# Performance work log

Hardware: AMD Instinct MI355X
Metric: run time of the kernel (lower is better)

The kernel has to match this reference:

```python
import jax, jax.numpy as jnp
import numpy as np
from jax import lax

BETA = 5.0
THRESHOLD = 20.0

def softplus5(x):
    # torch nn.Softplus(beta=5, threshold=20)
    return jnp.where(BETA * x > THRESHOLD, x, jax.nn.softplus(BETA * x) / BETA)

def setup_inputs() -> dict:
    key = jax.random.key(0)
    k1, k2, k3, k4, k5 = jax.random.split(key, 5)
    B, T, I, H = 128, 256, 1024, 1024
    stdv = 1.0 / np.sqrt(H)
    x = jax.random.normal(k1, (B, T, I), dtype=jnp.float32)
    hidden = jnp.zeros((2, B, H), dtype=jnp.float32)
    Wi = jax.random.uniform(k2, (H, I), dtype=jnp.float32, minval=-stdv, maxval=stdv)
    bi = jax.random.uniform(k3, (H,), dtype=jnp.float32, minval=-stdv, maxval=stdv)
    Wh = jax.random.uniform(k4, (H, H), dtype=jnp.float32, minval=-stdv, maxval=stdv)
    bh = jax.random.uniform(k5, (H,), dtype=jnp.float32, minval=-stdv, maxval=stdv)
    return {"x": x, "hidden": hidden, "Wi": Wi, "bi": bi, "Wh": Wh, "bh": bh}

def reference(x, hidden, Wi, bi, Wh, bh):
    # x: [B, T, I] (batch_first) -> time-major [T, B, I]
    xt = jnp.swapaxes(x, 0, 1)
    T = xt.shape[0]
    # precompute i2h for all steps (one big GEMM)
    pre = jnp.einsum('tbi,hi->tbh', xt, Wi) + bi  # [T, B, H]

    def step(h, p):
        h_next = softplus5(p + h @ Wh.T + bh)
        return h_next, h_next

    _, fwd = lax.scan(step, hidden[0], pre)          # fwd[t]: hidden after step t
    _, bwd = lax.scan(step, hidden[1], pre[::-1])    # bwd[j]: backward hidden at time i = T-1-j
    # bi_outputs appended for i = T-1 ... 0: position t holds cat(outputs[(T-1-t)-16], bwd[t])
    idx = (jnp.arange(T)[::-1] - 16) % T  # Python negative-index wrap of outputs[i-16]
    out = jnp.concatenate([fwd[idx], bwd], axis=-1)  # [T, B, 2H]
    return jnp.swapaxes(out, 0, 1)                   # [B, T, 2H]
```

## Files before the change

### kernel.cpp

```cpp
#include <hip/hip_runtime.h>
#include <stddef.h>

using short8 = __attribute__((ext_vector_type(8))) short;
using f32x4  = __attribute__((ext_vector_type(4))) float;
using f32x16 = __attribute__((ext_vector_type(16))) float;
using u16x4  = __attribute__((ext_vector_type(4))) unsigned short;
using u64    = unsigned long long;

__device__ __forceinline__ unsigned short cvt_bf16(float f) {
    unsigned u = __builtin_bit_cast(unsigned, f);
    u += 0x7fffu + ((u >> 16) & 1u);
    return (unsigned short)(u >> 16);
}

__device__ __forceinline__ void gload_lds16(const void* g, void* l) {
    __builtin_amdgcn_global_load_lds(
        (const __attribute__((address_space(1))) unsigned*)g,
        (__attribute__((address_space(3))) unsigned*)l, 16, 0, 0);
}

#define AL32(p)    __hip_atomic_load((p), __ATOMIC_RELAXED, __HIP_MEMORY_SCOPE_AGENT)
#define AS32(p, v) __hip_atomic_store((p), (v), __ATOMIC_RELAXED, __HIP_MEMORY_SCOPE_AGENT)

#define MFMA16(a, b, c) __builtin_amdgcn_mfma_f32_16x16x32_bf16((a), (b), (c), 0, 0, 0)
#define MFMA32(a, b, c) __builtin_amdgcn_mfma_f32_32x32x16_bf16((a), (b), (c), 0, 0, 0)


__global__ __launch_bounds__(256) void convert_w(const float* __restrict__ Wi,
                                                 const float* __restrict__ Wh,
                                                 unsigned short* __restrict__ Wib,
                                                 unsigned short* __restrict__ Whb) {
    const float* src = blockIdx.y ? Wh : Wi;
    unsigned short* dst = blockIdx.y ? Whb : Wib;
    int base = blockIdx.x * 2048 + threadIdx.x * 8;
#pragma unroll
    for (int c = 0; c < 2; ++c) {
        float4 v = *(const float4*)(src + base + c * 4);
        u16x4 o;
        o.x = cvt_bf16(v.x); o.y = cvt_bf16(v.y); o.z = cvt_bf16(v.z); o.w = cvt_bf16(v.w);
        *(u16x4*)(dst + base + c * 4) = o;
    }
}

__global__ __launch_bounds__(256) void init_h(const float* __restrict__ hidden,
                                              unsigned short* __restrict__ h0,
                                              unsigned* __restrict__ flags) {
    int row = blockIdx.x;
    int tid = threadIdx.x;
    float4 v = *(const float4*)(hidden + (size_t)row * 1024 + tid * 4);
    u16x4 o;
    o.x = cvt_bf16(v.x); o.y = cvt_bf16(v.y); o.z = cvt_bf16(v.z); o.w = cvt_bf16(v.w);
    *(u16x4*)(h0 + (size_t)row * 1024 + tid * 4) = o;
    if (tid < 64) flags[(size_t)row * 64 + tid] = 0;
}

__global__ __launch_bounds__(256) void pre_gemm(const float* __restrict__ x,
                                                const unsigned short* __restrict__ Wib,
                                                const float* __restrict__ bi,
                                                float* __restrict__ pre) {
    __shared__ unsigned short Alds[128 * 64];
    __shared__ unsigned short Blds[128 * 64];
    const int tid  = threadIdx.x;
    const int lane = tid & 63, wid = tid >> 6;
    const int wr = wid >> 1, wc = wid & 1;
    const int t  = blockIdx.y;
    const int n0 = blockIdx.x * 128;

    f32x4 acc[4][4] = {};

    for (int kt = 0; kt < 16; ++kt) {
        const int k0 = kt * 64;
        __syncthreads();
#pragma unroll
        for (int c = 0; c < 8; ++c) {
            int flat = c * 256 + tid;
            int row = flat >> 4;
            int seg = flat & 15;
            float4 v = *(const float4*)(x + (size_t)row * 262144 + (size_t)t * 1024 + k0 + seg * 4);
            u16x4 h;
            h.x = cvt_bf16(v.x); h.y = cvt_bf16(v.y); h.z = cvt_bf16(v.z); h.w = cvt_bf16(v.w);
            *(u16x4*)&Alds[row * 64 + seg * 4] = h;
        }
#pragma unroll
        for (int c = 0; c < 4; ++c) {
            int flat = c * 256 + tid;
            int row = flat >> 3;
            int seg = flat & 7;
            gload_lds16(Wib + (size_t)(n0 + row) * 1024 + k0 + seg * 8, &Blds[flat * 8]);
        }
        __syncthreads();
#pragma unroll
        for (int ks = 0; ks < 2; ++ks) {
            short8 a[4], b[4];
#pragma unroll
            for (int i = 0; i < 4; ++i)
                a[i] = *(const short8*)&Alds[(wr * 64 + i * 16 + (lane & 15)) * 64 + ks * 32 + (lane >> 4) * 8];
#pragma unroll
            for (int j = 0; j < 4; ++j)
                b[j] = *(const short8*)&Blds[(wc * 64 + j * 16 + (lane & 15)) * 64 + ks * 32 + (lane >> 4) * 8];
#pragma unroll
            for (int i = 0; i < 4; ++i)
#pragma unroll
                for (int j = 0; j < 4; ++j)
                    acc[i][j] = MFMA16(a[i], b[j], acc[i][j]);
        }
    }
    const int rbase = wr * 64 + (lane >> 4) * 4;
    const int cbase = n0 + wc * 64 + (lane & 15);
#pragma unroll
    for (int i = 0; i < 4; ++i) {
#pragma unroll
        for (int j = 0; j < 4; ++j) {
            int n = cbase + j * 16;
            float bv = bi[n];
#pragma unroll
            for (int r = 0; r < 4; ++r) {
                int m = rbase + i * 16 + r;
                pre[((size_t)t * 128 + m) * 1024 + n] = acc[i][j][r] + bv;
            }
        }
    }
}

__global__ __launch_bounds__(256, 1) void rnn_scan(const unsigned short* __restrict__ Whb,
                                                   const float* __restrict__ pre,
                                                   const float* __restrict__ bh,
                                                   unsigned short* __restrict__ ha,
                                                   unsigned short* __restrict__ hb,
                                                   float* __restrict__ out,
                                                   unsigned* __restrict__ flags) {
    __shared__ unsigned short Alds[32 * 1024];
    __shared__ float Red[4][1024];

    const int tid  = threadIdx.x;
    const int lane = tid & 63, wid = tid >> 6;
    const int bid  = blockIdx.x;
    const int g    = bid & 7, ni = bid >> 3;
    const int m0   = g * 32, n0 = ni * 32;
    const bool fwd = (g < 4);

    short8 bfrag[16];
    {
        const unsigned short* bp = Whb + (size_t)(n0 + (lane & 31)) * 1024
                                 + wid * 256 + (lane >> 5) * 8;
#pragma unroll
        for (int ks = 0; ks < 16; ++ks)
            bfrag[ks] = *(const short8*)(bp + ks * 16);
    }

    const int mloc = tid >> 3;
    const int nloc = (tid & 7) * 4;
    const int mg   = m0 + mloc;
    const int b    = mg & 127;
    const int n    = n0 + nloc;
    const f32x4 bh4 = *(const f32x4*)(bh + n);
    const float* prebase = pre + (size_t)b * 1024 + n;
    float* outp          = out + (size_t)b * 524288 + (fwd ? 0 : 1024) + n;

    const int   colswz = tid * 8;
    const char* arow   = (const char*)Alds + (lane & 31) * 2048;
    const int   aswz   = (lane & 15) << 4;
    const int   kb0    = wid * 512 + (lane >> 5) * 16;

    const unsigned* pf0 = flags + (size_t)(g * 32 + (lane & 31)) * 64 + (lane >> 5);
    const unsigned* pf1 = pf0 + 2;
    unsigned* myflag = flags + (size_t)(g * 32 + ni) * 64 + wid;

    for (int s = 0; s < 256; ++s) {
        const unsigned short* hin = (s & 1) ? hb : ha;
        unsigned short* hout      = (s & 1) ? ha : hb;
        const int prow = fwd ? s : 255 - s;

        const f32x4 pv = *(const f32x4*)(prebase + (size_t)prow * 131072);

        if (s > 0) {
            int fuel = 1 << 22;
            unsigned va, vb;
            do {
                va = AL32(pf0);
                vb = AL32(pf1);
            } while (!__all((int)(va >= (unsigned)s && vb >= (unsigned)s)) && --fuel);
        }

        {
            const u64* hsrc = (const u64*)(hin + (size_t)m0 * 1024);
            u64 tmp[32];
#pragma unroll
            for (int i = 0; i < 32; ++i)
                tmp[i] = __hip_atomic_load(&hsrc[(size_t)i * 256 + tid],
                                           __ATOMIC_RELAXED, __HIP_MEMORY_SCOPE_AGENT);
#pragma unroll
            for (int i = 0; i < 32; ++i)
                *(u64*)((char*)Alds + i * 2048 + (colswz ^ ((i & 15) << 4))) = tmp[i];
        }
        __syncthreads();

        f32x16 acc0 = {}, acc1 = {};
#pragma unroll
        for (int ks = 0; ks < 16; ++ks) {
            short8 a = *(const short8*)(arow + ((kb0 + ks * 32) ^ aswz));
            if (ks & 1) acc1 = MFMA32(a, bfrag[ks], acc1);
            else        acc0 = MFMA32(a, bfrag[ks], acc0);
        }
        f32x16 acc = acc0 + acc1;
#pragma unroll
        for (int r = 0; r < 16; ++r) {
            int row = (r & 3) + 8 * (r >> 2) + 4 * (lane >> 5);
            Red[wid][row * 32 + (lane & 31)] = acc[r];
        }
        __syncthreads();

        f32x4 ov;
        {
            const int o = tid * 4;
            f32x4 q0 = *(const f32x4*)&Red[0][o];
            f32x4 q1 = *(const f32x4*)&Red[1][o];
            f32x4 q2 = *(const f32x4*)&Red[2][o];
            f32x4 q3 = *(const f32x4*)&Red[3][o];
            f32x4 vv = q0 + q1 + q2 + q3 + pv + bh4;
            u16x4 hh;
#pragma unroll
            for (int j = 0; j < 4; ++j) {
                float xv = vv[j];
                float hv = (5.0f * xv > 20.0f) ? xv : 0.2f * log1pf(__expf(5.0f * xv));
                ov[j] = hv;
                hh[j] = cvt_bf16(hv);
            }
            __hip_atomic_store((u64*)(hout + (size_t)mg * 1024 + n),
                               __builtin_bit_cast(u64, hh),
                               __ATOMIC_RELAXED, __HIP_MEMORY_SCOPE_AGENT);
        }
        asm volatile("s_waitcnt vmcnt(0)" ::: "memory");
        if (lane == 0 && s < 255)
            AS32(myflag, (unsigned)(s + 1));

        const int tout = fwd ? ((239 - s) & 255) : s;
        __builtin_nontemporal_store(ov, (f32x4*)(outp + (size_t)tout * 2048));
    }
}

extern "C" void kernel_launch(void* const* d_in, const int* in_sizes, int n_in,
                              void* d_out, int out_size, void* d_ws, size_t ws_size,
                              hipStream_t stream) {
    const float* x      = (const float*)d_in[0];
    const float* hidden = (const float*)d_in[1];
    const float* Wi     = (const float*)d_in[2];
    const float* bi     = (const float*)d_in[3];
    const float* Wh     = (const float*)d_in[4];
    const float* bh     = (const float*)d_in[5];
    float* out = (float*)d_out;

    char* ws = (char*)d_ws;
    float*          pre = (float*)ws;
    unsigned short* Wib = (unsigned short*)(ws + 134217728);
    unsigned short* Whb = (unsigned short*)(ws + 136314880);
    unsigned short* ha  = (unsigned short*)(ws + 138412032);
    unsigned short* hb  = (unsigned short*)(ws + 138936320);
    unsigned*     flags = (unsigned*)(ws + 139460608);

    convert_w<<<dim3(512, 2), 256, 0, stream>>>(Wi, Wh, Wib, Whb);
    init_h<<<256, 256, 0, stream>>>(hidden, ha, flags);
    pre_gemm<<<dim3(8, 256), 256, 0, stream>>>(x, Wib, bi, pre);
    rnn_scan<<<256, 256, 0, stream>>>(Whb, pre, bh, ha, hb, out, flags);
}
```

Measured before the change: 1.355 ms.

## Wave-local h loads with compact flag layout and double-buffered reduction

Each wave now loads only the K-slice of the hidden state it consumes, using 16-byte inline-asm loads that bypass the caches, and writes that slice to its own LDS columns. This lets the per-step __syncthreads before the MFMA loop be replaced by local waitcnts. The reduction buffer is double-buffered by step parity so the next step's writes cannot race readers of the current step. The flags are packed into a dense 128-entry region per group so each lane polls a single word instead of two strided ones. The risk is correctness across waves, since each wave's A reads must stay within its own loaded columns and rows.

Measured after the change: 1.691 ms. 1.25x slower.

```diff
diff --git a/kernel.cpp b/kernel.cpp
--- a/kernel.cpp
+++ b/kernel.cpp
@@ -5,6 +5,7 @@
 using f32x4  = __attribute__((ext_vector_type(4))) float;
 using f32x16 = __attribute__((ext_vector_type(16))) float;
 using u16x4  = __attribute__((ext_vector_type(4))) unsigned short;
+using u32x4  = __attribute__((ext_vector_type(4))) unsigned;
 using u64    = unsigned long long;
 
 __device__ __forceinline__ unsigned short cvt_bf16(float f) {
@@ -51,7 +52,9 @@
     u16x4 o;
     o.x = cvt_bf16(v.x); o.y = cvt_bf16(v.y); o.z = cvt_bf16(v.z); o.w = cvt_bf16(v.w);
     *(u16x4*)(h0 + (size_t)row * 1024 + tid * 4) = o;
-    if (tid < 64) flags[(size_t)row * 64 + tid] = 0;
+    if (blockIdx.x == 0) {
+        for (int i = tid; i < 1024; i += 256) flags[i] = 0;
+    }
 }
 
 __global__ __launch_bounds__(256) void pre_gemm(const float* __restrict__ x,
@@ -130,7 +133,7 @@
                                                    float* __restrict__ out,
                                                    unsigned* __restrict__ flags) {
     __shared__ unsigned short Alds[32 * 1024];
-    __shared__ float Red[4][1024];
+    __shared__ float Red[2][4][1024];
 
     const int tid  = threadIdx.x;
     const int lane = tid & 63, wid = tid >> 6;
@@ -157,14 +160,14 @@
     const float* prebase = pre + (size_t)b * 1024 + n;
     float* outp          = out + (size_t)b * 524288 + (fwd ? 0 : 1024) + n;
 
-    const int   colswz = tid * 8;
-    const char* arow   = (const char*)Alds + (lane & 31) * 2048;
-    const int   aswz   = (lane & 15) << 4;
-    const int   kb0    = wid * 512 + (lane >> 5) * 16;
-
-    const unsigned* pf0 = flags + (size_t)(g * 32 + (lane & 31)) * 64 + (lane >> 5);
-    const unsigned* pf1 = pf0 + 2;
-    unsigned* myflag = flags + (size_t)(g * 32 + ni) * 64 + wid;
+    const int gcol  = wid * 512 + (lane & 31) * 16;
+    const int grow0 = lane >> 5;
+    const char* arow = (const char*)Alds + (lane & 31) * 2048;
+    const int   aswz = (lane & 15) << 4;
+    const int   kb0  = wid * 512 + (lane >> 5) * 16;
+
+    const unsigned* pollp = flags + g * 128 + (wid * 8 + ((lane >> 2) & 7)) * 4 + (lane & 3);
+    unsigned* pubp        = flags + g * 128 + ni * 4 + wid;
 
     for (int s = 0; s < 256; ++s) {
         const unsigned short* hin = (s & 1) ? hb : ha;
@@ -175,25 +178,31 @@
 
         if (s > 0) {
             int fuel = 1 << 22;
-            unsigned va, vb;
+            unsigned v;
             do {
-                va = AL32(pf0);
-                vb = AL32(pf1);
-            } while (!__all((int)(va >= (unsigned)s && vb >= (unsigned)s)) && --fuel);
+                v = AL32(pollp);
+            } while (!__all((int)(v >= (unsigned)s)) && --fuel);
         }
 
         {
-            const u64* hsrc = (const u64*)(hin + (size_t)m0 * 1024);
-            u64 tmp[32];
-#pragma unroll
-            for (int i = 0; i < 32; ++i)
-                tmp[i] = __hip_atomic_load(&hsrc[(size_t)i * 256 + tid],
-                                           __ATOMIC_RELAXED, __HIP_MEMORY_SCOPE_AGENT);
-#pragma unroll
-            for (int i = 0; i < 32; ++i)
-                *(u64*)((char*)Alds + i * 2048 + (colswz ^ ((i & 15) << 4))) = tmp[i];
-        }
-        __syncthreads();
+            const char* hsrc = (const char*)(hin + (size_t)m0 * 1024) + gcol;
+            u32x4 tmp[16];
+#pragma unroll
+            for (int i = 0; i < 16; ++i)
+                asm volatile("global_load_dwordx4 %0, %1, off sc0 sc1"
+                             : "=v"(tmp[i])
+                             : "v"(hsrc + (size_t)(grow0 + 2 * i) * 2048)
+                             : "memory");
+            asm volatile("s_waitcnt vmcnt(0)" ::: "memory");
+            __builtin_amdgcn_sched_barrier(0);
+#pragma unroll
+            for (int i = 0; i < 16; ++i) {
+                int r = grow0 + 2 * i;
+                *(u32x4*)((char*)Alds + r * 2048 + (gcol ^ ((r & 15) << 4))) = tmp[i];
+            }
+        }
+        asm volatile("s_waitcnt lgkmcnt(0)" ::: "memory");
+        __builtin_amdgcn_sched_barrier(0);
 
         f32x16 acc0 = {}, acc1 = {};
 #pragma unroll
@@ -206,17 +215,17 @@
 #pragma unroll
         for (int r = 0; r < 16; ++r) {
             int row = (r & 3) + 8 * (r >> 2) + 4 * (lane >> 5);
-            Red[wid][row * 32 + (lane & 31)] = acc[r];
+            Red[s & 1][wid][row * 32 + (lane & 31)] = acc[r];
         }
         __syncthreads();
 
         f32x4 ov;
         {
             const int o = tid * 4;
-            f32x4 q0 = *(const f32x4*)&Red[0][o];
-            f32x4 q1 = *(const f32x4*)&Red[1][o];
-            f32x4 q2 = *(const f32x4*)&Red[2][o];
-            f32x4 q3 = *(const f32x4*)&Red[3][o];
+            f32x4 q0 = *(const f32x4*)&Red[s & 1][0][o];
+            f32x4 q1 = *(const f32x4*)&Red[s & 1][1][o];
+            f32x4 q2 = *(const f32x4*)&Red[s & 1][2][o];
+            f32x4 q3 = *(const f32x4*)&Red[s & 1][3][o];
             f32x4 vv = q0 + q1 + q2 + q3 + pv + bh4;
             u16x4 hh;
 #pragma unroll
@@ -232,7 +241,7 @@
         }
         asm volatile("s_waitcnt vmcnt(0)" ::: "memory");
         if (lane == 0 && s < 255)
-            AS32(myflag, (unsigned)(s + 1));
+            AS32(pubp, (unsigned)(s + 1));
 
         const int tout = fwd ? ((239 - s) & 255) : s;
         __builtin_nontemporal_store(ov, (f32x4*)(outp + (size_t)tout * 2048));
```
